# Performance work log

Measured on AMD Instinct MI355X. Metric: run time of the kernel, lower is better.

## Reference

```python
import jax, jax.numpy as jnp
import numpy as np

B, N, KNB, F, H = 1, 50000, 16, 128, 128
BN_EPS = 1e-3  # keras BatchNormalization default epsilon
ALPHA = 0.3    # keras LeakyReLU default negative slope


def setup_inputs() -> dict:
    key = jax.random.key(0)
    ks = jax.random.split(key, 14)
    s_in = 1.0 / np.sqrt(F)
    s_cat = 1.0 / np.sqrt(F + H)
    return {
        'embeddings': jax.random.normal(ks[0], (B, N, F), jnp.float32),
        'weights': jnp.zeros((1, 1), jnp.float32),  # unused in call_att
        'neighbor_set': jax.random.randint(ks[1], (B, N, KNB), 0, N),
        'Wq': jax.random.normal(ks[2], (F, H), jnp.float32) * s_in,
        'bq': jnp.zeros((H,), jnp.float32),
        'Wk': jax.random.normal(ks[3], (F, H), jnp.float32) * s_in,
        'bk': jnp.zeros((H,), jnp.float32),
        'Wv': jax.random.normal(ks[4], (F, H), jnp.float32) * s_in,
        'bv': jnp.zeros((H,), jnp.float32),
        'W1': jax.random.normal(ks[5], (F + H, H), jnp.float32) * s_cat,
        'b1': jnp.zeros((H,), jnp.float32),
        'gamma': 1.0 + 0.1 * jax.random.normal(ks[6], (H,), jnp.float32),
        'beta': 0.1 * jax.random.normal(ks[7], (H,), jnp.float32),
        'mov_mean': 0.1 * jax.random.normal(ks[8], (H,), jnp.float32),
        'mov_var': 1.0 + 0.1 * jax.random.uniform(ks[9], (H,), jnp.float32),
    }


def reference(embeddings, weights, neighbor_set, Wq, bq, Wk, bk, Wv, bv,
              W1, b1, gamma, beta, mov_mean, mov_var):
    lrelu = lambda x: jax.nn.leaky_relu(x, ALPHA)
    # batched gather: nb[b, n, k] = embeddings[b, neighbor_set[b, n, k]]  -> [B,N,K,F]
    nb = jax.vmap(lambda e, idx: e[idx])(embeddings, neighbor_set)
    q = lrelu(embeddings @ Wq + bq)      # [B,N,H]
    k = lrelu(nb @ Wk + bk)              # [B,N,K,H]
    v = lrelu(nb @ Wv + bv)              # [B,N,K,H]
    # Q is tiled across the K neighbor rows in the original; every attention row
    # is identical, so mean-pool over rows == single-query attention. Same math.
    scores = jnp.einsum('bnh,bnkh->bnk', q, k)          # dot-product, no scale
    attn = jax.nn.softmax(scores, axis=-1)
    pooled = jnp.einsum('bnk,bnkh->bnh', attn, v)       # [B,N,H]
    h = lrelu(jnp.concatenate([embeddings, pooled], axis=-1) @ W1 + b1)
    h = h / (jnp.linalg.norm(h, axis=2, keepdims=True) + 1e-6)
    # BatchNormalization (inference form, axis=-1)
    return gamma * (h - mov_mean) * jax.lax.rsqrt(mov_var + BN_EPS) + beta
```

## Files before the change

kernel.cpp:

```cpp
#include <hip/hip_runtime.h>
#include <hip/hip_bf16.h>

#define N_NODES 50000
#define KNB 16
#define FDIM 128
#define HDIM 128
#define ALPHA 0.3f
#define BN_EPS 1e-3f

typedef __bf16 v8bf __attribute__((ext_vector_type(8)));
typedef float v4f __attribute__((ext_vector_type(4)));
typedef unsigned short ushort_t;

__device__ __forceinline__ float blo(unsigned int u) {
    union { float f; unsigned int i; } x; x.i = u << 16; return x.f;
}
__device__ __forceinline__ float bhi(unsigned int u) {
    union { float f; unsigned int i; } x; x.i = u & 0xffff0000u; return x.f;
}

__device__ __forceinline__ unsigned short f2bf(float f) {
    union { float f; unsigned int u; } x;
    x.f = f;
    unsigned int r = x.u + 0x7fffu + ((x.u >> 16) & 1u);
    return (unsigned short)(r >> 16);
}

__device__ __forceinline__ unsigned int pk2(float a, float b) {
    __hip_bfloat162 h = __float22bfloat162_rn(make_float2(a, b));
    union { __hip_bfloat162 h; unsigned int u; } r; r.h = h; return r.u;
}

__device__ __forceinline__ float lrelu(float x) { return x > 0.f ? x : ALPHA * x; }

__device__ __forceinline__ v8bf load8f(const float* p) {
    float4 A = ((const float4*)p)[0];
    float4 B = ((const float4*)p)[1];
    union { v8bf v; unsigned int u[4]; } r;
    r.u[0] = pk2(A.x, A.y); r.u[1] = pk2(A.z, A.w);
    r.u[2] = pk2(B.x, B.y); r.u[3] = pk2(B.z, B.w);
    return r.v;
}

__global__ __launch_bounds__(256) void prep_kernel(
    const float* __restrict__ Wq, const float* __restrict__ Wk,
    const float* __restrict__ Wv, const float* __restrict__ W1,
    ushort_t* __restrict__ WT)
{
    const int idx = blockIdx.x * 256 + threadIdx.x;
    if (idx < 16384) {
        int k = idx >> 7, n = idx & 127;
        WT[n * 128 + k] = f2bf(Wq[idx]);
    } else if (idx < 32768) {
        int i = idx - 16384; int k = i >> 7, n = i & 127;
        WT[16384 + n * 128 + k] = f2bf(Wk[i]);
    } else if (idx < 49152) {
        int i = idx - 32768; int k = i >> 7, n = i & 127;
        WT[32768 + n * 128 + k] = f2bf(Wv[i]);
    } else if (idx < 81920) {
        int i = idx - 49152; int k = i >> 7, n = i & 127;
        WT[49152 + n * 256 + k] = f2bf(W1[i]);
    }
}

#define QSTRIDE 560
#define KVSTRIDE 528
#define WTILE 18432

__global__ __launch_bounds__(256) void qkv_kernel(
    const float* __restrict__ E, const ushort_t* __restrict__ WT,
    const float* __restrict__ bq, const float* __restrict__ bk,
    const float* __restrict__ bv,
    float* __restrict__ Qo, ushort_t* __restrict__ KV)
{
    __shared__ char smem[4 * WTILE];

    const int tid  = threadIdx.x;
    const int wave = tid >> 6;
    const int lane = tid & 63;
    const int quad = lane >> 4;
    const int j    = lane & 15;
    const int row0 = blockIdx.x * 128 + wave * 32;

    char* const wbase = smem + wave * WTILE;

    const int ar0 = min(row0 + j,      N_NODES - 1);
    const int ar1 = min(row0 + 16 + j, N_NODES - 1);

    v8bf a0f[4], a1f[4];
#pragma unroll
    for (int ks = 0; ks < 4; ++ks) {
        const int k0 = ks * 32 + quad * 8;
        a0f[ks] = load8f(E + (size_t)ar0 * FDIM + k0);
        a1f[ks] = load8f(E + (size_t)ar1 * FDIM + k0);
    }

    const float* biases[3] = {bq, bk, bv};

    for (int w = 0; w < 3; ++w) {
        const ushort_t* __restrict__ Wsrc = WT + w * 16384;

        v4f acc[2][8];
#pragma unroll
        for (int rb = 0; rb < 2; ++rb)
#pragma unroll
            for (int c = 0; c < 8; ++c) acc[rb][c] = (v4f){0.f, 0.f, 0.f, 0.f};

#pragma unroll
        for (int ks = 0; ks < 4; ++ks) {
            const int k0 = ks * 32 + quad * 8;
            v8bf b[8];
#pragma unroll
            for (int c = 0; c < 8; ++c)
                b[c] = *(const v8bf*)(Wsrc + (c * 16 + j) * 128 + k0);
#pragma unroll
            for (int c = 0; c < 8; ++c) {
                acc[0][c] = __builtin_amdgcn_mfma_f32_16x16x32_bf16(b[c], a0f[ks], acc[0][c], 0, 0, 0);
                acc[1][c] = __builtin_amdgcn_mfma_f32_16x16x32_bf16(b[c], a1f[ks], acc[1][c], 0, 0, 0);
            }
        }

        const float* __restrict__ bias = biases[w];

        if (w == 0) {
#pragma unroll
            for (int rb = 0; rb < 2; ++rb)
#pragma unroll
                for (int c = 0; c < 8; ++c) {
                    const float4 bb = ((const float4*)bias)[c * 4 + quad];
                    v4f v = acc[rb][c];
                    v[0] = lrelu(v[0] + bb.x); v[1] = lrelu(v[1] + bb.y);
                    v[2] = lrelu(v[2] + bb.z); v[3] = lrelu(v[3] + bb.w);
                    *(v4f*)(wbase + (rb * 16 + j) * QSTRIDE + (c * 16 + quad * 4) * 4) = v;
                }
#pragma unroll
            for (int t = 0; t < 16; ++t) {
                const int r  = 2 * t + (lane >> 5);
                const v4f v  = *(const v4f*)(wbase + r * QSTRIDE + (lane & 31) * 16);
                const int gr = row0 + r;
                if (gr < N_NODES)
                    *(v4f*)(Qo + (size_t)gr * HDIM + (lane & 31) * 4) = v;
            }
        } else {
            const int voff = (w == 2) ? 256 : 0;
#pragma unroll
            for (int rb = 0; rb < 2; ++rb)
#pragma unroll
                for (int c = 0; c < 8; ++c) {
                    const float4 bb = ((const float4*)bias)[c * 4 + quad];
                    const v4f v = acc[rb][c];
                    uint2 u;
                    u.x = pk2(lrelu(v[0] + bb.x), lrelu(v[1] + bb.y));
                    u.y = pk2(lrelu(v[2] + bb.z), lrelu(v[3] + bb.w));
                    *(uint2*)(wbase + (rb * 16 + j) * KVSTRIDE + (c * 16 + quad * 4) * 2 + voff) = u;
                }
            if (w == 2) {
#pragma unroll
                for (int t = 0; t < 16; ++t) {
                    const int r  = 2 * t + (lane >> 5);
                    const uint4 v = *(const uint4*)(wbase + r * KVSTRIDE + (lane & 31) * 16);
                    const int gr = row0 + r;
                    if (gr < N_NODES)
                        *(uint4*)((char*)KV + (size_t)gr * 512 + (lane & 31) * 16) = v;
                }
            }
        }
    }
}

__global__ __launch_bounds__(256) void attn_kernel(
    float* __restrict__ QP, const ushort_t* __restrict__ KV,
    const int* __restrict__ nbr)
{
    const int tid  = threadIdx.x;
    const int wave = tid >> 6;
    const int lane = tid & 63;
    const int node = __builtin_amdgcn_readfirstlane(blockIdx.x * 4 + wave);

    const float2 qp = ((const float2*)(QP + (size_t)node * HDIM))[lane];

    int idxs[KNB];
    const int* nb = nbr + node * KNB;
#pragma unroll
    for (int t = 0; t < KNB; ++t) {
        int id = nb[t];
        idxs[t] = ((unsigned)id < (unsigned)N_NODES) ? id : 0;
    }

    float sc[KNB];
#pragma unroll
    for (int t = 0; t < KNB; ++t) {
        const unsigned int kp = ((const unsigned int*)(KV + (size_t)idxs[t] * 256))[lane];
        float p = qp.x * blo(kp) + qp.y * bhi(kp);
#pragma unroll
        for (int off = 32; off >= 1; off >>= 1) p += __shfl_xor(p, off, 64);
        sc[t] = p;
    }

    float m = sc[0];
#pragma unroll
    for (int t = 1; t < KNB; ++t) m = fmaxf(m, sc[t]);
    float s = 0.f;
#pragma unroll
    for (int t = 0; t < KNB; ++t) { sc[t] = __expf(sc[t] - m); s += sc[t]; }
    const float inv = 1.f / s;

    float p0 = 0.f, p1 = 0.f;
#pragma unroll
    for (int t = 0; t < KNB; ++t) {
        const unsigned int vp = ((const unsigned int*)(KV + (size_t)idxs[t] * 256 + 128))[lane];
        const float a = sc[t] * inv;
        p0 += a * blo(vp);
        p1 += a * bhi(vp);
    }

    ((float2*)(QP + (size_t)node * HDIM))[lane] = make_float2(p0, p1);
}

__global__ __launch_bounds__(256) void out_kernel(
    const float* __restrict__ E, const ushort_t* __restrict__ W1T,
    const float* __restrict__ b1,
    const float* __restrict__ gamma, const float* __restrict__ beta,
    const float* __restrict__ mmean, const float* __restrict__ mvar,
    float* __restrict__ OutP)
{
    __shared__ ushort_t sW[128 * 136];

    const int tid  = threadIdx.x;
    const int wave = tid >> 6;
    const int lane = tid & 63;
    const int quad = lane >> 4;
    const int j    = lane & 15;
    const int row0 = blockIdx.x * 128 + wave * 32;

    const int ar0 = min(row0 + j,      N_NODES - 1);
    const int ar1 = min(row0 + 16 + j, N_NODES - 1);

    v4f acc[2][8];
#pragma unroll
    for (int rb = 0; rb < 2; ++rb)
#pragma unroll
        for (int c = 0; c < 8; ++c) acc[rb][c] = (v4f){0.f, 0.f, 0.f, 0.f};

    for (int half = 0; half < 2; ++half) {
        for (int i = tid; i < 2048; i += 256) {
            int n = i >> 4, kc = i & 15;
            *(uint4*)(&sW[n * 136 + kc * 8]) =
                *(const uint4*)(W1T + n * 256 + half * 128 + kc * 8);
        }
        __syncthreads();

        const float* Abase = (half == 0) ? E : (const float*)OutP;
#pragma unroll
        for (int ks = 0; ks < 4; ++ks) {
            const int k0 = ks * 32 + quad * 8;
            v8bf a0 = load8f(Abase + (size_t)ar0 * 128 + k0);
            v8bf a1 = load8f(Abase + (size_t)ar1 * 128 + k0);
            v8bf b[8];
#pragma unroll
            for (int c = 0; c < 8; ++c)
                b[c] = *(const v8bf*)(&sW[(c * 16 + j) * 136 + k0]);
#pragma unroll
            for (int c = 0; c < 8; ++c) {
                acc[0][c] = __builtin_amdgcn_mfma_f32_16x16x32_bf16(a0, b[c], acc[0][c], 0, 0, 0);
                acc[1][c] = __builtin_amdgcn_mfma_f32_16x16x32_bf16(a1, b[c], acc[1][c], 0, 0, 0);
            }
        }
        __syncthreads();
    }

    float scale_[8], shift_[8], bias_[8];
#pragma unroll
    for (int c = 0; c < 8; ++c) {
        const int col = c * 16 + j;
        const float sc = gamma[col] * rsqrtf(mvar[col] + BN_EPS);
        scale_[c] = sc;
        shift_[c] = beta[col] - mmean[col] * sc;
        bias_[c]  = b1[col];
    }

#pragma unroll
    for (int rb = 0; rb < 2; ++rb)
#pragma unroll
        for (int c = 0; c < 8; ++c)
#pragma unroll
            for (int i = 0; i < 4; ++i)
                acc[rb][c][i] = lrelu(acc[rb][c][i] + bias_[c]);

#pragma unroll
    for (int rb = 0; rb < 2; ++rb) {
#pragma unroll
        for (int i = 0; i < 4; ++i) {
            float ss = 0.f;
#pragma unroll
            for (int c = 0; c < 8; ++c) ss += acc[rb][c][i] * acc[rb][c][i];
            ss += __shfl_xor(ss, 1, 64);
            ss += __shfl_xor(ss, 2, 64);
            ss += __shfl_xor(ss, 4, 64);
            ss += __shfl_xor(ss, 8, 64);
            const float invn = 1.f / (sqrtf(ss) + 1e-6f);
            const int r = row0 + rb * 16 + quad * 4 + i;
            if (r < N_NODES) {
#pragma unroll
                for (int c = 0; c < 8; ++c)
                    OutP[(size_t)r * HDIM + c * 16 + j] =
                        acc[rb][c][i] * invn * scale_[c] + shift_[c];
            }
        }
    }
}

extern "C" void kernel_launch(void* const* d_in, const int* in_sizes, int n_in,
                              void* d_out, int out_size, void* d_ws, size_t ws_size,
                              hipStream_t stream)
{
    const float* E     = (const float*)d_in[0];
    const int*   nbr   = (const int*)d_in[2];
    const float* Wq    = (const float*)d_in[3];
    const float* bq    = (const float*)d_in[4];
    const float* Wk    = (const float*)d_in[5];
    const float* bk    = (const float*)d_in[6];
    const float* Wv    = (const float*)d_in[7];
    const float* bv    = (const float*)d_in[8];
    const float* W1    = (const float*)d_in[9];
    const float* b1    = (const float*)d_in[10];
    const float* gam   = (const float*)d_in[11];
    const float* bet   = (const float*)d_in[12];
    const float* mmean = (const float*)d_in[13];
    const float* mvar  = (const float*)d_in[14];

    ushort_t* KV = (ushort_t*)d_ws;
    ushort_t* WT = KV + (size_t)N_NODES * 256;
    float* QP = (float*)d_out;

    const int gridA = (N_NODES + 127) / 128;
    prep_kernel<<<320, 256, 0, stream>>>(Wq, Wk, Wv, W1, WT);
    qkv_kernel<<<gridA, 256, 0, stream>>>(E, WT, bq, bk, bv, QP, KV);
    attn_kernel<<<N_NODES / 4, 256, 0, stream>>>(QP, KV, nbr);
    out_kernel<<<gridA, 256, 0, stream>>>(E, WT + 49152, b1, gam, bet, mmean, mvar, QP);
}
```

Before: 209.8 us.

## Vectorize attention gathers across lane groups and transpose MFMA output for vector stores

The attention kernel now splits the wave into four 16-lane groups, each handling one neighbor at a time with 16-byte loads. This cuts the number of serialized gather rounds and shortens the shuffle reductions, and the four groups are combined with cross-group shuffles. The output kernel swaps the MFMA operands so each lane holds four consecutive columns of one row, which allows float4 bias, BN-parameter loads and 16-byte output stores instead of scattered scalar stores. The cost is more registers and extra cross-group shuffles in the attention kernel.

```diff
diff --git a/kernel.cpp b/kernel.cpp
--- a/kernel.cpp
+++ b/kernel.cpp
@@ -168,6 +168,9 @@
     }
 }
 
+#define DOT8(kp) (q0.x*blo(kp.x) + q0.y*bhi(kp.x) + q0.z*blo(kp.y) + q0.w*bhi(kp.y) \
+                + q1.x*blo(kp.z) + q1.y*bhi(kp.z) + q1.z*blo(kp.w) + q1.w*bhi(kp.w))
+
 __global__ __launch_bounds__(256) void attn_kernel(
     float* __restrict__ QP, const ushort_t* __restrict__ KV,
     const int* __restrict__ nbr)
@@ -175,46 +178,85 @@
     const int tid  = threadIdx.x;
     const int wave = tid >> 6;
     const int lane = tid & 63;
+    const int grp  = lane >> 4;
+    const int li   = lane & 15;
     const int node = __builtin_amdgcn_readfirstlane(blockIdx.x * 4 + wave);
 
-    const float2 qp = ((const float2*)(QP + (size_t)node * HDIM))[lane];
-
-    int idxs[KNB];
+    const float4* qr = (const float4*)(QP + (size_t)node * HDIM + li * 8);
+    const float4 q0 = qr[0];
+    const float4 q1 = qr[1];
+
     const int* nb = nbr + node * KNB;
-#pragma unroll
-    for (int t = 0; t < KNB; ++t) {
-        int id = nb[t];
-        idxs[t] = ((unsigned)id < (unsigned)N_NODES) ? id : 0;
-    }
-
-    float sc[KNB];
-#pragma unroll
-    for (int t = 0; t < KNB; ++t) {
-        const unsigned int kp = ((const unsigned int*)(KV + (size_t)idxs[t] * 256))[lane];
-        float p = qp.x * blo(kp) + qp.y * bhi(kp);
-#pragma unroll
-        for (int off = 32; off >= 1; off >>= 1) p += __shfl_xor(p, off, 64);
-        sc[t] = p;
-    }
-
-    float m = sc[0];
-#pragma unroll
-    for (int t = 1; t < KNB; ++t) m = fmaxf(m, sc[t]);
-    float s = 0.f;
-#pragma unroll
-    for (int t = 0; t < KNB; ++t) { sc[t] = __expf(sc[t] - m); s += sc[t]; }
-    const float inv = 1.f / s;
-
-    float p0 = 0.f, p1 = 0.f;
-#pragma unroll
-    for (int t = 0; t < KNB; ++t) {
-        const unsigned int vp = ((const unsigned int*)(KV + (size_t)idxs[t] * 256 + 128))[lane];
-        const float a = sc[t] * inv;
-        p0 += a * blo(vp);
-        p1 += a * bhi(vp);
-    }
-
-    ((float2*)(QP + (size_t)node * HDIM))[lane] = make_float2(p0, p1);
+    int nid0, nid1, nid2, nid3;
+#pragma unroll
+    for (int t = 0; t < 4; ++t) {
+        int i0 = nb[t * 4 + 0]; i0 = ((unsigned)i0 < (unsigned)N_NODES) ? i0 : 0;
+        int i1 = nb[t * 4 + 1]; i1 = ((unsigned)i1 < (unsigned)N_NODES) ? i1 : 0;
+        int i2 = nb[t * 4 + 2]; i2 = ((unsigned)i2 < (unsigned)N_NODES) ? i2 : 0;
+        int i3 = nb[t * 4 + 3]; i3 = ((unsigned)i3 < (unsigned)N_NODES) ? i3 : 0;
+        int v = i0;
+        v = (grp == 1) ? i1 : v;
+        v = (grp == 2) ? i2 : v;
+        v = (grp == 3) ? i3 : v;
+        if (t == 0) nid0 = v; else if (t == 1) nid1 = v;
+        else if (t == 2) nid2 = v; else nid3 = v;
+    }
+
+    const char* kvb = (const char*)KV;
+    const size_t lo16 = (size_t)(li * 16);
+
+    const uint4 k0 = *(const uint4*)(kvb + (size_t)nid0 * 512 + lo16);
+    const uint4 k1 = *(const uint4*)(kvb + (size_t)nid1 * 512 + lo16);
+    const uint4 k2 = *(const uint4*)(kvb + (size_t)nid2 * 512 + lo16);
+    const uint4 k3 = *(const uint4*)(kvb + (size_t)nid3 * 512 + lo16);
+    float s0 = DOT8(k0), s1 = DOT8(k1), s2 = DOT8(k2), s3 = DOT8(k3);
+#pragma unroll
+    for (int off = 1; off <= 8; off <<= 1) {
+        s0 += __shfl_xor(s0, off, 64);
+        s1 += __shfl_xor(s1, off, 64);
+        s2 += __shfl_xor(s2, off, 64);
+        s3 += __shfl_xor(s3, off, 64);
+    }
+
+    float m = fmaxf(fmaxf(s0, s1), fmaxf(s2, s3));
+    m = fmaxf(m, __shfl_xor(m, 16, 64));
+    m = fmaxf(m, __shfl_xor(m, 32, 64));
+    s0 = __expf(s0 - m); s1 = __expf(s1 - m);
+    s2 = __expf(s2 - m); s3 = __expf(s3 - m);
+    float ssum = s0 + s1 + s2 + s3;
+    ssum += __shfl_xor(ssum, 16, 64);
+    ssum += __shfl_xor(ssum, 32, 64);
+    const float inv = 1.f / ssum;
+    const float a0 = s0 * inv, a1 = s1 * inv, a2 = s2 * inv, a3 = s3 * inv;
+
+    const uint4 v0 = *(const uint4*)(kvb + (size_t)nid0 * 512 + 256 + lo16);
+    const uint4 v1 = *(const uint4*)(kvb + (size_t)nid1 * 512 + 256 + lo16);
+    const uint4 v2 = *(const uint4*)(kvb + (size_t)nid2 * 512 + 256 + lo16);
+    const uint4 v3 = *(const uint4*)(kvb + (size_t)nid3 * 512 + 256 + lo16);
+
+    float p0 = a0 * blo(v0.x) + a1 * blo(v1.x) + a2 * blo(v2.x) + a3 * blo(v3.x);
+    float p1 = a0 * bhi(v0.x) + a1 * bhi(v1.x) + a2 * bhi(v2.x) + a3 * bhi(v3.x);
+    float p2 = a0 * blo(v0.y) + a1 * blo(v1.y) + a2 * blo(v2.y) + a3 * blo(v3.y);
+    float p3 = a0 * bhi(v0.y) + a1 * bhi(v1.y) + a2 * bhi(v2.y) + a3 * bhi(v3.y);
+    float p4 = a0 * blo(v0.z) + a1 * blo(v1.z) + a2 * blo(v2.z) + a3 * blo(v3.z);
+    float p5 = a0 * bhi(v0.z) + a1 * bhi(v1.z) + a2 * bhi(v2.z) + a3 * bhi(v3.z);
+    float p6 = a0 * blo(v0.w) + a1 * blo(v1.w) + a2 * blo(v2.w) + a3 * blo(v3.w);
+    float p7 = a0 * bhi(v0.w) + a1 * bhi(v1.w) + a2 * bhi(v2.w) + a3 * bhi(v3.w);
+
+    p0 += __shfl_xor(p0, 16, 64); p1 += __shfl_xor(p1, 16, 64);
+    p2 += __shfl_xor(p2, 16, 64); p3 += __shfl_xor(p3, 16, 64);
+    p4 += __shfl_xor(p4, 16, 64); p5 += __shfl_xor(p5, 16, 64);
+    p6 += __shfl_xor(p6, 16, 64); p7 += __shfl_xor(p7, 16, 64);
+    p0 += __shfl_xor(p0, 32, 64); p1 += __shfl_xor(p1, 32, 64);
+    p2 += __shfl_xor(p2, 32, 64); p3 += __shfl_xor(p3, 32, 64);
+    p4 += __shfl_xor(p4, 32, 64); p5 += __shfl_xor(p5, 32, 64);
+    p6 += __shfl_xor(p6, 32, 64); p7 += __shfl_xor(p7, 32, 64);
+
+    if (grp == 0) {
+        float4* out = (float4*)(QP + (size_t)node * HDIM + li * 8);
+        out[0] = make_float4(p0, p1, p2, p3);
+        out[1] = make_float4(p4, p5, p6, p7);
+    }
 }
 
 __global__ __launch_bounds__(256) void out_kernel(
@@ -262,50 +304,63 @@
                 b[c] = *(const v8bf*)(&sW[(c * 16 + j) * 136 + k0]);
 #pragma unroll
             for (int c = 0; c < 8; ++c) {
-                acc[0][c] = __builtin_amdgcn_mfma_f32_16x16x32_bf16(a0, b[c], acc[0][c], 0, 0, 0);
-                acc[1][c] = __builtin_amdgcn_mfma_f32_16x16x32_bf16(a1, b[c], acc[1][c], 0, 0, 0);
+                acc[0][c] = __builtin_amdgcn_mfma_f32_16x16x32_bf16(b[c], a0, acc[0][c], 0, 0, 0);
+                acc[1][c] = __builtin_amdgcn_mfma_f32_16x16x32_bf16(b[c], a1, acc[1][c], 0, 0, 0);
             }
         }
         __syncthreads();
     }
 
-    float scale_[8], shift_[8], bias_[8];
 #pragma unroll
     for (int c = 0; c < 8; ++c) {
-        const int col = c * 16 + j;
-        const float sc = gamma[col] * rsqrtf(mvar[col] + BN_EPS);
-        scale_[c] = sc;
-        shift_[c] = beta[col] - mmean[col] * sc;
-        bias_[c]  = b1[col];
-    }
-
-#pragma unroll
-    for (int rb = 0; rb < 2; ++rb)
-#pragma unroll
-        for (int c = 0; c < 8; ++c)
-#pragma unroll
-            for (int i = 0; i < 4; ++i)
-                acc[rb][c][i] = lrelu(acc[rb][c][i] + bias_[c]);
-
-#pragma unroll
-    for (int rb = 0; rb < 2; ++rb) {
+        const float4 bb = ((const float4*)b1)[c * 4 + quad];
+#pragma unroll
+        for (int rb = 0; rb < 2; ++rb) {
+            acc[rb][c][0] = lrelu(acc[rb][c][0] + bb.x);
+            acc[rb][c][1] = lrelu(acc[rb][c][1] + bb.y);
+            acc[rb][c][2] = lrelu(acc[rb][c][2] + bb.z);
+            acc[rb][c][3] = lrelu(acc[rb][c][3] + bb.w);
+        }
+    }
+
+    float ss0 = 0.f, ss1 = 0.f;
+#pragma unroll
+    for (int c = 0; c < 8; ++c)
 #pragma unroll
         for (int i = 0; i < 4; ++i) {
-            float ss = 0.f;
-#pragma unroll
-            for (int c = 0; c < 8; ++c) ss += acc[rb][c][i] * acc[rb][c][i];
-            ss += __shfl_xor(ss, 1, 64);
-            ss += __shfl_xor(ss, 2, 64);
-            ss += __shfl_xor(ss, 4, 64);
-            ss += __shfl_xor(ss, 8, 64);
-            const float invn = 1.f / (sqrtf(ss) + 1e-6f);
-            const int r = row0 + rb * 16 + quad * 4 + i;
-            if (r < N_NODES) {
-#pragma unroll
-                for (int c = 0; c < 8; ++c)
-                    OutP[(size_t)r * HDIM + c * 16 + j] =
-                        acc[rb][c][i] * invn * scale_[c] + shift_[c];
-            }
+            ss0 += acc[0][c][i] * acc[0][c][i];
+            ss1 += acc[1][c][i] * acc[1][c][i];
+        }
+    ss0 += __shfl_xor(ss0, 16, 64); ss1 += __shfl_xor(ss1, 16, 64);
+    ss0 += __shfl_xor(ss0, 32, 64); ss1 += __shfl_xor(ss1, 32, 64);
+    const float inv0 = 1.f / (sqrtf(ss0) + 1e-6f);
+    const float inv1 = 1.f / (sqrtf(ss1) + 1e-6f);
+
+    const int r0w = row0 + j;
+    const int r1w = row0 + 16 + j;
+#pragma unroll
+    for (int c = 0; c < 8; ++c) {
+        const float4 g4 = ((const float4*)gamma)[c * 4 + quad];
+        const float4 vv = ((const float4*)mvar )[c * 4 + quad];
+        const float4 be = ((const float4*)beta )[c * 4 + quad];
+        const float4 mm = ((const float4*)mmean)[c * 4 + quad];
+        v4f sc4, sh4;
+        sc4[0] = g4.x * rsqrtf(vv.x + BN_EPS); sh4[0] = be.x - mm.x * sc4[0];
+        sc4[1] = g4.y * rsqrtf(vv.y + BN_EPS); sh4[1] = be.y - mm.y * sc4[1];
+        sc4[2] = g4.z * rsqrtf(vv.z + BN_EPS); sh4[2] = be.z - mm.z * sc4[2];
+        sc4[3] = g4.w * rsqrtf(vv.w + BN_EPS); sh4[3] = be.w - mm.w * sc4[3];
+        const int colb = c * 16 + quad * 4;
+        if (r0w < N_NODES) {
+            v4f o;
+#pragma unroll
+            for (int i = 0; i < 4; ++i) o[i] = acc[0][c][i] * inv0 * sc4[i] + sh4[i];
+            *(v4f*)(OutP + (size_t)r0w * HDIM + colb) = o;
+        }
+        if (r1w < N_NODES) {
+            v4f o;
+#pragma unroll
+            for (int i = 0; i < 4; ++i) o[i] = acc[1][c][i] * inv1 * sc4[i] + sh4[i];
+            *(v4f*)(OutP + (size_t)r1w * HDIM + colb) = o;
         }
     }
 }
```

After: 212.1 us. No clear change (+1.1%).
